# Kernel tuning notes

Hardware: AMD Instinct MI355X
Metric: run time of the kernel (lower is better)

The kernel has to match this reference:

```python
import jax, jax.numpy as jnp
import numpy as np
import math

B, T, C, H = 2, 2048, 512, 8
TOPK = 64
HD = C // H
EPS = 1e-12  # torch F.normalize eps


def setup_inputs() -> dict:
    key = jax.random.key(0)
    ks = jax.random.split(key, 6)
    s = 1.0 / math.sqrt(C)
    q = jax.random.normal(ks[0], (B, T, C), dtype=jnp.float32)
    tgt_mask = jnp.tril(jnp.ones((T, T), dtype=jnp.float32)).reshape(1, 1, T, T)
    Wq = jax.random.normal(ks[1], (C, C), dtype=jnp.float32) * s
    Wk = jax.random.normal(ks[2], (C, C), dtype=jnp.float32) * s
    Wv = jax.random.normal(ks[3], (C, C), dtype=jnp.float32) * s
    Wp = jax.random.normal(ks[4], (C, C), dtype=jnp.float32) * s
    bq = jnp.zeros((C,), jnp.float32)
    bk = jnp.zeros((C,), jnp.float32)
    bv = jnp.zeros((C,), jnp.float32)
    bp = jnp.zeros((C,), jnp.float32)
    return {"q": q, "tgt_mask": tgt_mask, "Wq": Wq, "bq": bq, "Wk": Wk, "bk": bk,
            "Wv": Wv, "bv": bv, "Wp": Wp, "bp": bp}


def _attn(q, tgt_mask, Wq, bq, Wk, bk, Wv, bv, Wp, bp):
    Bt, Tt, Ct = q.shape
    # self-attention: k = v = q (module path when k, v are None)
    qh = (q @ Wq + bq).reshape(Bt, Tt, H, HD).transpose(0, 2, 1, 3)  # [B,H,T,hd]
    kh = (q @ Wk + bk).reshape(Bt, Tt, H, HD).transpose(0, 2, 1, 3)
    vh = (q @ Wv + bv).reshape(Bt, Tt, H, HD).transpose(0, 2, 1, 3)
    # L2-normalize v along head dim (F.normalize, p=2, eps=1e-12)
    vn = jnp.linalg.norm(vh, axis=-1, keepdims=True)
    vh = vh / jnp.maximum(vn, EPS)
    att = jnp.einsum('bhqd,bhkd->bhqk', qh, kh) * (1.0 / math.sqrt(HD))
    neg = -jnp.inf
    att = jnp.where(tgt_mask[:, :, :Tt, :Tt] == 0, neg, att)
    # top-k sparsification: drop entries strictly below the k-th largest per row
    top = jax.lax.top_k(att, TOPK)[0]            # [B,H,T,TOPK]
    vk = top[..., -1:]                            # k-th largest threshold
    att = jnp.where(att < vk, neg, att)
    att = jax.nn.softmax(att, axis=-1)
    y = jnp.einsum('bhqk,bhkd->bhqd', att, vh)
    y = y.transpose(0, 2, 1, 3).reshape(Bt, Tt, Ct)
    return y @ Wp + bp


def reference(q, tgt_mask, Wq, bq, Wk, bk, Wv, bv, Wp, bp):
    return _attn(q, tgt_mask, Wq, bq, Wk, bk, Wv, bv, Wp, bp)
```

## Files before the change

kernel.cpp:

```cpp
#include <hip/hip_runtime.h>
#include <cstdint>
#include <math.h>

static constexpr int Bc = 2, Tc = 2048, Cch = 512, Hc = 8;
static constexpr int BT = Bc * Tc;
static constexpr int NBH = Bc * Hc;
static constexpr int NRT = Tc / 128;
static constexpr int NTRI = NRT * (NRT + 1) / 2;
static constexpr size_t TRI_FLOATS = (size_t)NTRI * 16384;

typedef float f32x4 __attribute__((ext_vector_type(4)));
typedef short s16x8 __attribute__((ext_vector_type(8)));
typedef unsigned short u16x8 __attribute__((ext_vector_type(8)));
typedef unsigned short u16x4 __attribute__((ext_vector_type(4)));

__device__ __host__ inline constexpr int tri_i(int r) { return r * (r + 1) / 2; }

__device__ inline float wave_sum_f(float x) {
#pragma unroll
  for (int o = 32; o; o >>= 1) x += __shfl_xor(x, o);
  return x;
}
__device__ inline unsigned short f2bf(float x) {
  unsigned u = __float_as_uint(x);
  return (unsigned short)((u + 0x7FFFu + ((u >> 16) & 1u)) >> 16);
}
__device__ inline float bf2f(unsigned short h) { return __uint_as_float(((unsigned)h) << 16); }
__device__ inline float su2f(unsigned s) {
  unsigned u = (s & 0x80000000u) ? (s ^ 0x80000000u) : ~s;
  return __uint_as_float(u);
}

__global__ __launch_bounds__(256) void split_k(const float* __restrict__ X,
    unsigned short* __restrict__ hi, unsigned short* __restrict__ lo, int n8) {
  int i = blockIdx.x * 256 + threadIdx.x;
  if (i >= n8) return;
  const f32x4* p = (const f32x4*)X + (size_t)i * 2;
  f32x4 a = p[0], b = p[1];
  float v[8] = {a[0], a[1], a[2], a[3], b[0], b[1], b[2], b[3]};
  u16x8 h, l;
#pragma unroll
  for (int c = 0; c < 8; c++) {
    unsigned short hh = f2bf(v[c]);
    h[c] = hh;
    l[c] = f2bf(v[c] - bf2f(hh));
  }
  *(u16x8*)(hi + (size_t)i * 8) = h;
  *(u16x8*)(lo + (size_t)i * 8) = l;
}

__global__ __launch_bounds__(256) void splitT_k(const float* __restrict__ W,
    unsigned short* __restrict__ hiT, unsigned short* __restrict__ loT) {
  __shared__ float t[64][65];
  const int tid = threadIdx.x;
  const int k0 = blockIdx.x * 64, n0 = blockIdx.y * 64;
#pragma unroll
  for (int p = 0; p < 4; p++) {
    int idx = tid + p * 256, kk = idx >> 4, n4 = idx & 15;
    f32x4 v = *(const f32x4*)&W[(size_t)(k0 + kk) * Cch + n0 + n4 * 4];
    t[kk][n4 * 4 + 0] = v[0]; t[kk][n4 * 4 + 1] = v[1];
    t[kk][n4 * 4 + 2] = v[2]; t[kk][n4 * 4 + 3] = v[3];
  }
  __syncthreads();
  {
    int n = tid >> 2, ks = tid & 3;
    u16x8 h0, h1, l0, l1;
#pragma unroll
    for (int kk = 0; kk < 8; kk++) {
      float x = t[ks * 16 + kk][n];
      unsigned short hh = f2bf(x);
      h0[kk] = hh; l0[kk] = f2bf(x - bf2f(hh));
      float y = t[ks * 16 + 8 + kk][n];
      unsigned short hy = f2bf(y);
      h1[kk] = hy; l1[kk] = f2bf(y - bf2f(hy));
    }
    size_t base = (size_t)(n0 + n) * Cch + k0 + ks * 16;
    *(u16x8*)(hiT + base) = h0; *(u16x8*)(hiT + base + 8) = h1;
    *(u16x8*)(loT + base) = l0; *(u16x8*)(loT + base + 8) = l1;
  }
}

template <int BF16OUT>
__global__ __launch_bounds__(256) void gemm3_k(
    const unsigned short* __restrict__ Ahi, const unsigned short* __restrict__ Alo,
    const unsigned short* __restrict__ Bhi, const unsigned short* __restrict__ Blo,
    const float* __restrict__ bias, void* __restrict__ Out) {
  __shared__ unsigned short Ah[2][64][72];
  __shared__ unsigned short Bs[2][64][72];
  const int tid = threadIdx.x;
  const int w = tid >> 6, lane = tid & 63, e = lane >> 4, lr = lane & 15;
  const int wr = w >> 1, wc = w & 1;
  const int brow = blockIdx.y * 64, bcol = blockIdx.x * 64;
  f32x4 acc[2][2] = {};
  for (int k0 = 0; k0 < Cch; k0 += 64) {
#pragma unroll
    for (int p = 0; p < 2; p++) {
      int idx = tid + p * 256, row = idx >> 3, seg = idx & 7;
      *(u16x8*)&Ah[0][row][seg * 8] = *(const u16x8*)&Ahi[(size_t)(brow + row) * Cch + k0 + seg * 8];
      *(u16x8*)&Ah[1][row][seg * 8] = *(const u16x8*)&Alo[(size_t)(brow + row) * Cch + k0 + seg * 8];
      *(u16x8*)&Bs[0][row][seg * 8] = *(const u16x8*)&Bhi[(size_t)(bcol + row) * Cch + k0 + seg * 8];
      *(u16x8*)&Bs[1][row][seg * 8] = *(const u16x8*)&Blo[(size_t)(bcol + row) * Cch + k0 + seg * 8];
    }
    __syncthreads();
#pragma unroll
    for (int ks = 0; ks < 2; ks++) {
      s16x8 ah[2], al[2], bh[2], bl[2];
#pragma unroll
      for (int ti = 0; ti < 2; ti++) {
        ah[ti] = *(const s16x8*)&Ah[0][wr * 32 + ti * 16 + lr][ks * 32 + e * 8];
        al[ti] = *(const s16x8*)&Ah[1][wr * 32 + ti * 16 + lr][ks * 32 + e * 8];
      }
#pragma unroll
      for (int tj = 0; tj < 2; tj++) {
        bh[tj] = *(const s16x8*)&Bs[0][wc * 32 + tj * 16 + lr][ks * 32 + e * 8];
        bl[tj] = *(const s16x8*)&Bs[1][wc * 32 + tj * 16 + lr][ks * 32 + e * 8];
      }
#pragma unroll
      for (int ti = 0; ti < 2; ti++)
#pragma unroll
        for (int tj = 0; tj < 2; tj++) {
          acc[ti][tj] = __builtin_amdgcn_mfma_f32_16x16x32_bf16(ah[ti], bh[tj], acc[ti][tj], 0, 0, 0);
          acc[ti][tj] = __builtin_amdgcn_mfma_f32_16x16x32_bf16(ah[ti], bl[tj], acc[ti][tj], 0, 0, 0);
          acc[ti][tj] = __builtin_amdgcn_mfma_f32_16x16x32_bf16(al[ti], bh[tj], acc[ti][tj], 0, 0, 0);
        }
    }
    __syncthreads();
  }
#pragma unroll
  for (int ti = 0; ti < 2; ti++)
#pragma unroll
    for (int tj = 0; tj < 2; tj++) {
      int col = bcol + wc * 32 + tj * 16 + lr;
      float bi = bias[col];
#pragma unroll
      for (int r = 0; r < 4; r++) {
        int row = brow + wr * 32 + ti * 16 + e * 4 + r;
        float v = acc[ti][tj][r] + bi;
        if (BF16OUT) ((unsigned short*)Out)[(size_t)row * Cch + col] = f2bf(v);
        else         ((float*)Out)[(size_t)row * Cch + col] = v;
      }
    }
}

__global__ __launch_bounds__(256) void vnormt_k(const float* __restrict__ Vf,
                                                unsigned short* __restrict__ Vt) {
  __shared__ unsigned short T[64][72];
  const int tid = threadIdx.x;
  const int t0 = blockIdx.x * 64;
  const int h = blockIdx.y;
  const int tok = tid >> 2;
  const int q = tid & 3;
  const float* src = Vf + (size_t)(t0 + tok) * Cch + h * 64 + q * 16;
  f32x4 v[4];
  float ss = 0.f;
#pragma unroll
  for (int i = 0; i < 4; i++) {
    v[i] = *(const f32x4*)(src + i * 4);
#pragma unroll
    for (int c = 0; c < 4; c++) ss += v[i][c] * v[i][c];
  }
  ss += __shfl_xor(ss, 1);
  ss += __shfl_xor(ss, 2);
  float inv = 1.0f / fmaxf(sqrtf(ss), 1e-12f);
#pragma unroll
  for (int i = 0; i < 4; i++)
#pragma unroll
    for (int c = 0; c < 4; c++)
      T[q * 16 + i * 4 + c][tok] = f2bf(v[i][c] * inv);
  __syncthreads();
  const int d = tid >> 2, s2 = (tid & 3) * 2;
  const int b = t0 >> 11;
  size_t base = ((size_t)((b * Hc + h) * 64 + d)) * Tc + (t0 & 2047);
  *(u16x8*)(Vt + base + s2 * 8)     = *(const u16x8*)&T[d][s2 * 8];
  *(u16x8*)(Vt + base + s2 * 8 + 8) = *(const u16x8*)&T[d][s2 * 8 + 8];
}

__global__ __launch_bounds__(512) void sqk_k(const unsigned short* __restrict__ Qp,
    const unsigned short* __restrict__ Kp, float* __restrict__ S, int bh0) {
  __shared__ unsigned short Qs[128][72], Ks[128][72];
  int rt, ct;
  {
    int i = blockIdx.x;
    int r = (int)((sqrtf(8.f * i + 1.f) - 1.f) * 0.5f);
    while ((r + 1) * (r + 2) / 2 <= i) r++;
    while (r * (r + 1) / 2 > i) r--;
    rt = r; ct = i - r * (r + 1) / 2;
  }
  const int bh = bh0 + blockIdx.y, b = bh >> 3, h = bh & 7;
  const int tid = threadIdx.x, w = tid >> 6, lane = tid & 63, e = lane >> 4, lr = lane & 15;
#pragma unroll
  for (int p = 0; p < 2; p++) {
    int idx = tid + p * 512, row = idx >> 3, seg = idx & 7;
    *(u16x8*)&Qs[row][seg * 8] = *(const u16x8*)&Qp[((size_t)(b * Tc + rt * 128 + row)) * Cch + h * 64 + seg * 8];
    *(u16x8*)&Ks[row][seg * 8] = *(const u16x8*)&Kp[((size_t)(b * Tc + ct * 128 + row)) * Cch + h * 64 + seg * 8];
  }
  __syncthreads();
  f32x4 acc[8] = {};
  s16x8 a[2];
#pragma unroll
  for (int ks = 0; ks < 2; ks++) a[ks] = *(const s16x8*)&Qs[w * 16 + lr][ks * 32 + e * 8];
#pragma unroll
  for (int tj = 0; tj < 8; tj++) {
#pragma unroll
    for (int ks = 0; ks < 2; ks++) {
      s16x8 bb = *(const s16x8*)&Ks[tj * 16 + lr][ks * 32 + e * 8];
      acc[tj] = __builtin_amdgcn_mfma_f32_16x16x32_bf16(a[ks], bb, acc[tj], 0, 0, 0);
    }
  }
  float* Srow0 = S + (size_t)(bh - bh0) * TRI_FLOATS + (size_t)tri_i(rt) * 16384;
  const int stride = (rt + 1) * 128;
#pragma unroll
  for (int tj = 0; tj < 8; tj++)
#pragma unroll
    for (int r = 0; r < 4; r++) {
      int row = w * 16 + e * 4 + r;
      Srow0[(size_t)row * stride + ct * 128 + tj * 16 + lr] = acc[tj][r] * 0.125f;
    }
}

__global__ __launch_bounds__(512, 4) void sel_k(float* __restrict__ S) {
  int wid = blockIdx.x * 8 + (threadIdx.x >> 6);
  int lane = threadIdx.x & 63;
  int bhl = wid >> 11, t = wid & 2047;
  int rt = t >> 7, lrow = t & 127;
  int stride = (rt + 1) * 128;
  float* row = S + (size_t)bhl * TRI_FLOATS + (size_t)tri_i(rt) * 16384 + (size_t)lrow * stride;
  unsigned su[32];
#pragma unroll
  for (int c = 0; c < 8; c++) {
    if (c * 256 < stride) {
      int j0 = c * 256 + lane * 4;
      f32x4 v;
      if (j0 < stride) v = *(const f32x4*)(row + j0);
      else { v[0] = v[1] = v[2] = v[3] = -INFINITY; }
#pragma unroll
      for (int cc = 0; cc < 4; cc++) {
        float x = (j0 + cc <= t) ? v[cc] : -INFINITY;
        unsigned u = __float_as_uint(x);
        su[c * 4 + cc] = (u & 0x80000000u) ? ~u : (u | 0x80000000u);
      }
    } else {
#pragma unroll
      for (int cc = 0; cc < 4; cc++) su[c * 4 + cc] = 0x007FFFFFu;
    }
  }
  unsigned lo = 0;
#pragma unroll 1
  for (int bit = 31; bit >= 0; bit--) {
    unsigned cand = lo | (1u << bit);
    int cnt = 0;
#pragma unroll
    for (int c = 0; c < 8; c++)
      if (c * 256 < stride)
#pragma unroll
        for (int q = 0; q < 4; q++)
          cnt += (int)__popcll(__ballot(su[c * 4 + q] >= cand));
    if (cnt >= 64) {
      lo = cand;
      if (cnt == 64) {
        unsigned mn = 0xFFFFFFFFu;
#pragma unroll
        for (int c = 0; c < 8; c++)
          if (c * 256 < stride)
#pragma unroll
            for (int q = 0; q < 4; q++) { unsigned x = (su[c * 4 + q] >= cand) ? su[c * 4 + q] : 0xFFFFFFFFu; mn = mn < x ? mn : x; }
#pragma unroll
        for (int o = 32; o; o >>= 1) { unsigned x = (unsigned)__shfl_xor((int)mn, o); mn = mn < x ? mn : x; }
        lo = mn;
        break;
      }
    }
  }
  unsigned mx = 0;
#pragma unroll
  for (int c = 0; c < 8; c++)
    if (c * 256 < stride)
#pragma unroll
      for (int q = 0; q < 4; q++) mx = mx > su[c * 4 + q] ? mx : su[c * 4 + q];
#pragma unroll
  for (int o = 32; o; o >>= 1) { unsigned x = (unsigned)__shfl_xor((int)mx, o); mx = mx > x ? mx : x; }
  float m = su2f(mx);
  float sum = 0.f;
#pragma unroll
  for (int c = 0; c < 8; c++)
    if (c * 256 < stride)
#pragma unroll
      for (int q = 0; q < 4; q++) {
        float v = su2f(su[c * 4 + q]);
        float wv = (su[c * 4 + q] >= lo) ? __expf(v - m) : 0.f;
        su[c * 4 + q] = __float_as_uint(wv);
        sum += wv;
      }
  sum = wave_sum_f(sum);
  float inv = 1.f / sum;
  unsigned short* prow = (unsigned short*)row;
#pragma unroll
  for (int c = 0; c < 8; c++) {
    if (c * 256 < stride) {
      int j0 = c * 256 + lane * 4;
      if (j0 < stride) {
        u16x4 pk;
#pragma unroll
        for (int cc = 0; cc < 4; cc++) pk[cc] = f2bf(__uint_as_float(su[c * 4 + cc]) * inv);
        *(u16x4*)(prow + j0) = pk;
      }
    }
  }
}

__global__ __launch_bounds__(512) void pv_k(const float* __restrict__ S,
    const unsigned short* __restrict__ Vt,
    unsigned short* __restrict__ Yhi, unsigned short* __restrict__ Ylo, int bh0) {
  __shared__ unsigned short Ps[128][136];
  __shared__ unsigned short Vs[64][136];
  const int rt = blockIdx.x, bh = bh0 + blockIdx.y, b = bh >> 3, h = bh & 7;
  const int tid = threadIdx.x, w = tid >> 6, lane = tid & 63, e = lane >> 4, lr = lane & 15;
  const int stride = (rt + 1) * 128;
  const float* Srow0 = S + (size_t)(bh - bh0) * TRI_FLOATS + (size_t)tri_i(rt) * 16384;
  f32x4 acc[4] = {};
  for (int kt = 0; kt <= rt; kt++) {
#pragma unroll
    for (int p = 0; p < 4; p++) {
      int idx = tid + p * 512, row = idx >> 4, seg = idx & 15;
      const unsigned short* src = (const unsigned short*)(Srow0 + (size_t)row * stride) + kt * 128 + seg * 8;
      *(u16x8*)&Ps[row][seg * 8] = *(const u16x8*)src;
    }
#pragma unroll
    for (int p = 0; p < 2; p++) {
      int idx = tid + p * 512, d = idx >> 4, seg = idx & 15;
      *(u16x8*)&Vs[d][seg * 8] = *(const u16x8*)&Vt[((size_t)(bh * 64 + d)) * Tc + kt * 128 + seg * 8];
    }
    __syncthreads();
#pragma unroll
    for (int ks = 0; ks < 4; ks++) {
      s16x8 a = *(const s16x8*)&Ps[w * 16 + lr][ks * 32 + e * 8];
#pragma unroll
      for (int tj = 0; tj < 4; tj++) {
        s16x8 bb = *(const s16x8*)&Vs[tj * 16 + lr][ks * 32 + e * 8];
        acc[tj] = __builtin_amdgcn_mfma_f32_16x16x32_bf16(a, bb, acc[tj], 0, 0, 0);
      }
    }
    __syncthreads();
  }
#pragma unroll
  for (int tj = 0; tj < 4; tj++)
#pragma unroll
    for (int r = 0; r < 4; r++) {
      int row = rt * 128 + w * 16 + e * 4 + r;
      size_t g = ((size_t)(b * Tc + row)) * Cch + h * 64 + tj * 16 + lr;
      float y = acc[tj][r];
      unsigned short hh = f2bf(y);
      Yhi[g] = hh;
      Ylo[g] = f2bf(y - bf2f(hh));
    }
}

extern "C" void kernel_launch(void* const* d_in, const int* in_sizes, int n_in,
                              void* d_out, int out_size, void* d_ws, size_t ws_size,
                              hipStream_t stream) {
  const float* q  = (const float*)d_in[0];
  const float* Wq = (const float*)d_in[2];
  const float* bq = (const float*)d_in[3];
  const float* Wk = (const float*)d_in[4];
  const float* bk = (const float*)d_in[5];
  const float* Wv = (const float*)d_in[6];
  const float* bv = (const float*)d_in[7];
  const float* Wp = (const float*)d_in[8];
  const float* bp = (const float*)d_in[9];
  float* out = (float*)d_out;
  char* ws = (char*)d_ws;
  constexpr size_t MB = 1u << 20;

  unsigned short* qhi = (unsigned short*)(ws + 0 * MB);
  unsigned short* qlo = (unsigned short*)(ws + 4 * MB);
  unsigned short* Qp  = (unsigned short*)(ws + 8 * MB);
  unsigned short* Kp  = (unsigned short*)(ws + 12 * MB);
  unsigned short* Vt  = (unsigned short*)(ws + 16 * MB);
  unsigned short* wsp = (unsigned short*)(ws + 20 * MB);
  float* Sb = (float*)(ws + 24 * MB);
  float* Vf = (float*)(ws + 24 * MB);
  unsigned short* Yhi = qhi;
  unsigned short* Ylo = qlo;
  auto WT = [&](int i) { return wsp + (size_t)i * 262144; };

  int nbh = NBH;
  while (nbh > 1 && 24 * MB + TRI_FLOATS * 4 * (size_t)nbh > ws_size) nbh >>= 1;

  split_k<<<(BT * Cch / 8 + 255) / 256, 256, 0, stream>>>(q, qhi, qlo, BT * Cch / 8);
  dim3 g8(8, 8);
  splitT_k<<<g8, 256, 0, stream>>>(Wq, WT(0), WT(1));
  splitT_k<<<g8, 256, 0, stream>>>(Wk, WT(2), WT(3));
  splitT_k<<<g8, 256, 0, stream>>>(Wv, WT(4), WT(5));
  splitT_k<<<g8, 256, 0, stream>>>(Wp, WT(6), WT(7));

  dim3 gp(Cch / 64, BT / 64);
  gemm3_k<1><<<gp, 256, 0, stream>>>(qhi, qlo, WT(0), WT(1), bq, Qp);
  gemm3_k<1><<<gp, 256, 0, stream>>>(qhi, qlo, WT(2), WT(3), bk, Kp);
  gemm3_k<0><<<gp, 256, 0, stream>>>(qhi, qlo, WT(4), WT(5), bv, Vf);
  vnormt_k<<<dim3(BT / 64, Hc), 256, 0, stream>>>(Vf, Vt);

  for (int c = 0; c < NBH / nbh; c++) {
    int bh0 = c * nbh;
    sqk_k<<<dim3(NTRI, nbh), 512, 0, stream>>>(Qp, Kp, Sb, bh0);
    sel_k<<<nbh * 256, 512, 0, stream>>>(Sb);
    pv_k<<<dim3(NRT, nbh), 512, 0, stream>>>(Sb, Vt, Yhi, Ylo, bh0);
  }

  gemm3_k<0><<<gp, 256, 0, stream>>>(Yhi, Ylo, WT(6), WT(7), bp, out);
}
```

Baseline: 226.4 us.

## Batch weight splits and QKV GEMMs into single launches, rebalance PV and selection

The four weight split-transpose launches become one launch using a z grid dimension. The three QKV projection GEMMs become one launch over a z dimension, with 512-thread blocks and 128-row tiles; the output projection uses the same wider tile. pv_k now splits each 128-row tile into two 64-row halves and schedules the longest causal tiles first. sel_k also walks its blocks in reverse so the longest rows start first. The aim is fewer kernel launches and less tail imbalance from the triangular workload, at the cost of more shared memory per GEMM block and more redundant V tile loads in pv_k.

```diff
diff --git a/kernel.cpp b/kernel.cpp
--- a/kernel.cpp
+++ b/kernel.cpp
@@ -49,8 +49,13 @@
   *(u16x8*)(lo + (size_t)i * 8) = l;
 }
 
-__global__ __launch_bounds__(256) void splitT_k(const float* __restrict__ W,
-    unsigned short* __restrict__ hiT, unsigned short* __restrict__ loT) {
+__global__ __launch_bounds__(256) void splitT4_k(const float* __restrict__ Wq,
+    const float* __restrict__ Wk, const float* __restrict__ Wv,
+    const float* __restrict__ Wp, unsigned short* __restrict__ wsp) {
+  const int z = blockIdx.z;
+  const float* W = (z == 0) ? Wq : (z == 1) ? Wk : (z == 2) ? Wv : Wp;
+  unsigned short* hiT = wsp + (size_t)z * 524288;
+  unsigned short* loT = hiT + 262144;
   __shared__ float t[64][65];
   const int tid = threadIdx.x;
   const int k0 = blockIdx.x * 64, n0 = blockIdx.y * 64;
@@ -80,24 +85,28 @@
   }
 }
 
-template <int BF16OUT>
-__global__ __launch_bounds__(256) void gemm3_k(
+template <int QKV>
+__device__ inline void gemm3w_body(
     const unsigned short* __restrict__ Ahi, const unsigned short* __restrict__ Alo,
     const unsigned short* __restrict__ Bhi, const unsigned short* __restrict__ Blo,
-    const float* __restrict__ bias, void* __restrict__ Out) {
-  __shared__ unsigned short Ah[2][64][72];
+    const float* __restrict__ bias, void* __restrict__ Out0, int z,
+    unsigned short* Qp, unsigned short* Kp, float* Vf) {
+  __shared__ unsigned short Ah[2][128][72];
   __shared__ unsigned short Bs[2][64][72];
   const int tid = threadIdx.x;
   const int w = tid >> 6, lane = tid & 63, e = lane >> 4, lr = lane & 15;
   const int wr = w >> 1, wc = w & 1;
-  const int brow = blockIdx.y * 64, bcol = blockIdx.x * 64;
+  const int brow = blockIdx.y * 128, bcol = blockIdx.x * 64;
   f32x4 acc[2][2] = {};
   for (int k0 = 0; k0 < Cch; k0 += 64) {
 #pragma unroll
     for (int p = 0; p < 2; p++) {
-      int idx = tid + p * 256, row = idx >> 3, seg = idx & 7;
+      int idx = tid + p * 512, row = idx >> 3, seg = idx & 7;
       *(u16x8*)&Ah[0][row][seg * 8] = *(const u16x8*)&Ahi[(size_t)(brow + row) * Cch + k0 + seg * 8];
       *(u16x8*)&Ah[1][row][seg * 8] = *(const u16x8*)&Alo[(size_t)(brow + row) * Cch + k0 + seg * 8];
+    }
+    {
+      int row = tid >> 3, seg = tid & 7;
       *(u16x8*)&Bs[0][row][seg * 8] = *(const u16x8*)&Bhi[(size_t)(bcol + row) * Cch + k0 + seg * 8];
       *(u16x8*)&Bs[1][row][seg * 8] = *(const u16x8*)&Blo[(size_t)(bcol + row) * Cch + k0 + seg * 8];
     }
@@ -136,10 +145,35 @@
       for (int r = 0; r < 4; r++) {
         int row = brow + wr * 32 + ti * 16 + e * 4 + r;
         float v = acc[ti][tj][r] + bi;
-        if (BF16OUT) ((unsigned short*)Out)[(size_t)row * Cch + col] = f2bf(v);
-        else         ((float*)Out)[(size_t)row * Cch + col] = v;
-      }
-    }
+        size_t g = (size_t)row * Cch + col;
+        if (QKV) {
+          if (z == 0) Qp[g] = f2bf(v);
+          else if (z == 1) Kp[g] = f2bf(v);
+          else Vf[g] = v;
+        } else {
+          ((float*)Out0)[g] = v;
+        }
+      }
+    }
+}
+
+__global__ __launch_bounds__(512) void gemm3w_qkv_k(
+    const unsigned short* __restrict__ Ahi, const unsigned short* __restrict__ Alo,
+    const unsigned short* __restrict__ wsp,
+    const float* __restrict__ bq, const float* __restrict__ bk, const float* __restrict__ bv,
+    unsigned short* __restrict__ Qp, unsigned short* __restrict__ Kp, float* __restrict__ Vf) {
+  const int z = blockIdx.z;
+  const unsigned short* Bhi = wsp + (size_t)z * 524288;
+  const unsigned short* Blo = Bhi + 262144;
+  const float* bias = (z == 0) ? bq : (z == 1) ? bk : bv;
+  gemm3w_body<1>(Ahi, Alo, Bhi, Blo, bias, nullptr, z, Qp, Kp, Vf);
+}
+
+__global__ __launch_bounds__(512) void gemm3w_out_k(
+    const unsigned short* __restrict__ Ahi, const unsigned short* __restrict__ Alo,
+    const unsigned short* __restrict__ Bhi, const unsigned short* __restrict__ Blo,
+    const float* __restrict__ bias, float* __restrict__ Out) {
+  gemm3w_body<0>(Ahi, Alo, Bhi, Blo, bias, Out, 0, nullptr, nullptr, nullptr);
 }
 
 __global__ __launch_bounds__(256) void vnormt_k(const float* __restrict__ Vf,
@@ -219,7 +253,8 @@
 }
 
 __global__ __launch_bounds__(512, 4) void sel_k(float* __restrict__ S) {
-  int wid = blockIdx.x * 8 + (threadIdx.x >> 6);
+  int bidr = (int)gridDim.x - 1 - (int)blockIdx.x;
+  int wid = bidr * 8 + (threadIdx.x >> 6);
   int lane = threadIdx.x & 63;
   int bhl = wid >> 11, t = wid & 2047;
   int rt = t >> 7, lrow = t & 127;
@@ -311,43 +346,45 @@
 __global__ __launch_bounds__(512) void pv_k(const float* __restrict__ S,
     const unsigned short* __restrict__ Vt,
     unsigned short* __restrict__ Yhi, unsigned short* __restrict__ Ylo, int bh0) {
-  __shared__ unsigned short Ps[128][136];
+  __shared__ unsigned short Ps[64][136];
   __shared__ unsigned short Vs[64][136];
-  const int rt = blockIdx.x, bh = bh0 + blockIdx.y, b = bh >> 3, h = bh & 7;
+  const int x = blockIdx.x;
+  const int rt = NRT - 1 - (x >> 1);
+  const int half = x & 1;
+  const int bh = bh0 + blockIdx.y, b = bh >> 3, h = bh & 7;
   const int tid = threadIdx.x, w = tid >> 6, lane = tid & 63, e = lane >> 4, lr = lane & 15;
   const int stride = (rt + 1) * 128;
+  const int rbase = half * 64;
   const float* Srow0 = S + (size_t)(bh - bh0) * TRI_FLOATS + (size_t)tri_i(rt) * 16384;
-  f32x4 acc[4] = {};
+  const int rg = w & 3, dh = w >> 2;
+  f32x4 acc[2] = {};
   for (int kt = 0; kt <= rt; kt++) {
 #pragma unroll
-    for (int p = 0; p < 4; p++) {
-      int idx = tid + p * 512, row = idx >> 4, seg = idx & 15;
-      const unsigned short* src = (const unsigned short*)(Srow0 + (size_t)row * stride) + kt * 128 + seg * 8;
-      *(u16x8*)&Ps[row][seg * 8] = *(const u16x8*)src;
-    }
-#pragma unroll
     for (int p = 0; p < 2; p++) {
-      int idx = tid + p * 512, d = idx >> 4, seg = idx & 15;
-      *(u16x8*)&Vs[d][seg * 8] = *(const u16x8*)&Vt[((size_t)(bh * 64 + d)) * Tc + kt * 128 + seg * 8];
+      int idx = tid + p * 512, pr = idx >> 4, seg = idx & 15;
+      const unsigned short* src =
+          (const unsigned short*)(Srow0 + (size_t)(rbase + pr) * stride) + kt * 128 + seg * 8;
+      *(u16x8*)&Ps[pr][seg * 8] = *(const u16x8*)src;
+      *(u16x8*)&Vs[pr][seg * 8] = *(const u16x8*)&Vt[((size_t)(bh * 64 + pr)) * Tc + kt * 128 + seg * 8];
     }
     __syncthreads();
 #pragma unroll
     for (int ks = 0; ks < 4; ks++) {
-      s16x8 a = *(const s16x8*)&Ps[w * 16 + lr][ks * 32 + e * 8];
-#pragma unroll
-      for (int tj = 0; tj < 4; tj++) {
-        s16x8 bb = *(const s16x8*)&Vs[tj * 16 + lr][ks * 32 + e * 8];
+      s16x8 a = *(const s16x8*)&Ps[rg * 16 + lr][ks * 32 + e * 8];
+#pragma unroll
+      for (int tj = 0; tj < 2; tj++) {
+        s16x8 bb = *(const s16x8*)&Vs[dh * 32 + tj * 16 + lr][ks * 32 + e * 8];
         acc[tj] = __builtin_amdgcn_mfma_f32_16x16x32_bf16(a, bb, acc[tj], 0, 0, 0);
       }
     }
     __syncthreads();
   }
 #pragma unroll
-  for (int tj = 0; tj < 4; tj++)
+  for (int tj = 0; tj < 2; tj++)
 #pragma unroll
     for (int r = 0; r < 4; r++) {
-      int row = rt * 128 + w * 16 + e * 4 + r;
-      size_t g = ((size_t)(b * Tc + row)) * Cch + h * 64 + tj * 16 + lr;
+      int row = rt * 128 + rbase + rg * 16 + e * 4 + r;
+      size_t g = ((size_t)(b * Tc + row)) * Cch + h * 64 + dh * 32 + tj * 16 + lr;
       float y = acc[tj][r];
       unsigned short hh = f2bf(y);
       Yhi[g] = hh;
@@ -381,30 +418,24 @@
   float* Vf = (float*)(ws + 24 * MB);
   unsigned short* Yhi = qhi;
   unsigned short* Ylo = qlo;
-  auto WT = [&](int i) { return wsp + (size_t)i * 262144; };
 
   int nbh = NBH;
   while (nbh > 1 && 24 * MB + TRI_FLOATS * 4 * (size_t)nbh > ws_size) nbh >>= 1;
 
   split_k<<<(BT * Cch / 8 + 255) / 256, 256, 0, stream>>>(q, qhi, qlo, BT * Cch / 8);
-  dim3 g8(8, 8);
-  splitT_k<<<g8, 256, 0, stream>>>(Wq, WT(0), WT(1));
-  splitT_k<<<g8, 256, 0, stream>>>(Wk, WT(2), WT(3));
-  splitT_k<<<g8, 256, 0, stream>>>(Wv, WT(4), WT(5));
-  splitT_k<<<g8, 256, 0, stream>>>(Wp, WT(6), WT(7));
-
-  dim3 gp(Cch / 64, BT / 64);
-  gemm3_k<1><<<gp, 256, 0, stream>>>(qhi, qlo, WT(0), WT(1), bq, Qp);
-  gemm3_k<1><<<gp, 256, 0, stream>>>(qhi, qlo, WT(2), WT(3), bk, Kp);
-  gemm3_k<0><<<gp, 256, 0, stream>>>(qhi, qlo, WT(4), WT(5), bv, Vf);
+  splitT4_k<<<dim3(8, 8, 4), 256, 0, stream>>>(Wq, Wk, Wv, Wp, wsp);
+
+  gemm3w_qkv_k<<<dim3(Cch / 64, BT / 128, 3), 512, 0, stream>>>(
+      qhi, qlo, wsp, bq, bk, bv, Qp, Kp, Vf);
   vnormt_k<<<dim3(BT / 64, Hc), 256, 0, stream>>>(Vf, Vt);
 
   for (int c = 0; c < NBH / nbh; c++) {
     int bh0 = c * nbh;
     sqk_k<<<dim3(NTRI, nbh), 512, 0, stream>>>(Qp, Kp, Sb, bh0);
     sel_k<<<nbh * 256, 512, 0, stream>>>(Sb);
-    pv_k<<<dim3(NRT, nbh), 512, 0, stream>>>(Sb, Vt, Yhi, Ylo, bh0);
-  }
-
-  gemm3_k<0><<<gp, 256, 0, stream>>>(Yhi, Ylo, WT(6), WT(7), bp, out);
-}
+    pv_k<<<dim3(2 * NRT, nbh), 512, 0, stream>>>(Sb, Vt, Yhi, Ylo, bh0);
+  }
+
+  gemm3w_out_k<<<dim3(Cch / 64, BT / 128), 512, 0, stream>>>(
+      Yhi, Ylo, wsp + (size_t)6 * 262144, wsp + (size_t)7 * 262144, bp, out);
+}
```

Result: faster. 205.8 us (-9.1%).
